# Kernel optimization log

Hardware: AMD Instinct MI355X
Metric: run time of the kernel (lower is better)

## Reference

```python
import jax, jax.numpy as jnp
import numpy as np

B, S, D, DK = 8, 2048, 768, 214
DROPOUT_P = 0.1


def setup_inputs() -> dict:
    key = jax.random.key(0)
    ks = jax.random.split(key, 11)
    x1 = jax.random.normal(ks[0], (B, S, D), jnp.float32)
    x2 = jax.random.normal(ks[1], (B, S, D), jnp.float32)
    x3 = jax.random.normal(ks[2], (B, S, D), jnp.float32)
    Wq = jax.random.normal(ks[3], (DK, D), jnp.float32) * (1.0 / np.sqrt(D))
    bq = jax.random.normal(ks[4], (DK,), jnp.float32) * 0.01
    Wk = jax.random.normal(ks[5], (DK, D), jnp.float32) * (1.0 / np.sqrt(D))
    bk = jax.random.normal(ks[6], (DK,), jnp.float32) * 0.01
    Wv = jax.random.normal(ks[7], (D, D), jnp.float32) * (1.0 / np.sqrt(D))
    bv = jax.random.normal(ks[8], (D,), jnp.float32) * 0.01
    # full-tensor elementwise divisor: uniform(0,1) + 1, as in the source
    inv_scale = jax.random.uniform(ks[9], (S, S), jnp.float32) + 1.0
    # deterministic inverted-dropout mask, keep prob = 1 - p
    keep = 1.0 - DROPOUT_P
    dropout_mask = (jax.random.uniform(ks[10], (B, S, S)) < keep).astype(jnp.float32) / keep
    return dict(x1=x1, x2=x2, x3=x3, Wq=Wq, bq=bq, Wk=Wk, bk=bk,
                Wv=Wv, bv=bv, inv_scale=inv_scale, dropout_mask=dropout_mask)


def reference(x1, x2, x3, Wq, bq, Wk, bk, Wv, bv, inv_scale, dropout_mask):
    q = jnp.einsum('bsd,kd->bsk', x1, Wq) + bq          # [B,S,DK]
    k = jnp.einsum('bsd,kd->bsk', x2, Wk) + bk          # [B,S,DK]
    v = jnp.einsum('bsd,ed->bse', x3, Wv) + bv          # [B,S,D]
    attn = jnp.einsum('bsk,btk->bst', q, k)             # [B,S,S]
    scaled = attn / inv_scale                           # elementwise full-tensor divisor
    p = jax.nn.softmax(scaled, axis=-1) * dropout_mask  # softmax + inverted dropout
    return jnp.einsum('bst,btd->bsd', p, v)             # [B,S,D]
```

## Files before the change

### kernel.cpp

```cpp
#include <hip/hip_runtime.h>
#include <hip/hip_bf16.h>

typedef unsigned short ushort;
typedef short bf16x8 __attribute__((ext_vector_type(8)));
typedef float f32x4 __attribute__((ext_vector_type(4)));

#define NB 8
#define SS 2048
#define DD 768
#define DKV 214
#define DKP 224
#define WROWS 256
#define MSHIFT 40.0f

__device__ __forceinline__ float bf2f(ushort u) {
  union { unsigned int i; float f; } v; v.i = ((unsigned int)u) << 16; return v.f;
}
__device__ __forceinline__ ushort f2bf(float f) {
  union { float f; unsigned int i; } v; v.f = f;
  unsigned int x = v.i;
  return (ushort)((x + 0x7fffu + ((x >> 16) & 1u)) >> 16);
}
__device__ __forceinline__ void split8v(f32x4 a, f32x4 b, bf16x8& h, bf16x8& l) {
#pragma unroll
  for (int j = 0; j < 4; ++j) {
    ushort h0 = f2bf(a[j]); h[j]     = (short)h0; l[j]     = (short)f2bf(a[j] - bf2f(h0));
    ushort h1 = f2bf(b[j]); h[j + 4] = (short)h1; l[j + 4] = (short)f2bf(b[j] - bf2f(h1));
  }
}
__device__ __forceinline__ bf16x8 cvt8v(f32x4 a, f32x4 b) {
  bf16x8 r;
#pragma unroll
  for (int j = 0; j < 4; ++j) { r[j] = (short)f2bf(a[j]); r[j + 4] = (short)f2bf(b[j]); }
  return r;
}
__device__ __forceinline__ void gload16(const void* g, void* l) {
  __builtin_amdgcn_global_load_lds(
      (const __attribute__((address_space(1))) void*)g,
      (__attribute__((address_space(3))) void*)l, 16, 0, 0);
}

__global__ __launch_bounds__(256)
void prep_w(const float* __restrict__ Wq, const float* __restrict__ Wk,
            const float* __restrict__ Wv,
            ushort* __restrict__ Wqh, ushort* __restrict__ Wql,
            ushort* __restrict__ Wkh, ushort* __restrict__ Wkl,
            ushort* __restrict__ Wvb, float* __restrict__ Z)
{
  const int NW = WROWS * DD;
  const int NV = DD * DD;
  for (int i = blockIdx.x * 256 + threadIdx.x; i < NB * SS; i += gridDim.x * 256)
    Z[i] = 0.f;
  for (int i = blockIdx.x * 256 + threadIdx.x; i < 2 * NW + NV; i += gridDim.x * 256) {
    if (i < NW) {
      int r = i / DD, c = i % DD;
      float v = (r < DKV) ? Wq[i] : 0.f;
      ushort h = f2bf(v);
      int d = (c >> 5) * (WROWS * 32) + r * 32 + (c & 31);
      Wqh[d] = h; Wql[d] = f2bf(v - bf2f(h));
    } else if (i < 2 * NW) {
      int j = i - NW;
      int r = j / DD, c = j % DD;
      float v = (r < DKV) ? Wk[j] : 0.f;
      ushort h = f2bf(v);
      int d = (c >> 5) * (WROWS * 32) + r * 32 + (c & 31);
      Wkh[d] = h; Wkl[d] = f2bf(v - bf2f(h));
    } else {
      int j = i - 2 * NW;
      int r = j / DD, c = j % DD;
      Wvb[(c >> 5) * (DD * 32) + r * 32 + (c & 31)] = f2bf(Wv[j]);
    }
  }
}

__global__ __launch_bounds__(256, 4)
void gemm_qk(const float* __restrict__ x1, const float* __restrict__ x2,
             const ushort* __restrict__ Wqh, const ushort* __restrict__ Wql,
             const ushort* __restrict__ Wkh, const ushort* __restrict__ Wkl,
             const float* __restrict__ bq, const float* __restrict__ bk,
             ushort* __restrict__ Qph, ushort* __restrict__ Qpl,
             ushort* __restrict__ Kph, ushort* __restrict__ Kpl)
{
  const int m0 = blockIdx.x * 64;
  const int which = blockIdx.y >> 1;
  const int n0 = (blockIdx.y & 1) * 128;
  const int tid = threadIdx.x;
  const int w  = tid >> 6;
  const int l  = tid & 63;
  const int lr = l & 15;
  const int lh = l >> 4;

  const float*  A    = which ? x2 : x1;
  const ushort* Bh   = which ? Wkh : Wqh;
  const ushort* Bl   = which ? Wkl : Wql;
  const float*  bias = which ? bk : bq;
  ushort* Ch = which ? Kph : Qph;
  ushort* Cl = which ? Kpl : Qpl;

  __shared__ __align__(16) char lds[2][2][128][64];

  const int srow = (w << 4) + (l >> 2);
  const size_t gc = (size_t)srow * 64 + (size_t)((((l & 3) ^ ((srow >> 1) & 3))) << 4);
  const char* gbh = (const char*)Bh + (size_t)n0 * 64;
  const char* gbl = (const char*)Bl + (size_t)n0 * 64;

  const f32x4 fzero = {0.f, 0.f, 0.f, 0.f};
  f32x4 acc[8];
#pragma unroll
  for (int nt = 0; nt < 8; ++nt) acc[nt] = fzero;

  const float* arow = A + (size_t)(m0 + w * 16 + lr) * DD + lh * 8;

#define QKSTAGE(buf, kk) do {                                             \
    size_t ko = (size_t)(kk) * (WROWS * 64);                              \
    gload16(gbh + ko + gc,        &lds[buf][0][w << 4][0]);               \
    gload16(gbh + ko + gc + 4096, &lds[buf][0][(w << 4) + 64][0]);        \
    gload16(gbl + ko + gc,        &lds[buf][1][w << 4][0]);               \
    gload16(gbl + ko + gc + 4096, &lds[buf][1][(w << 4) + 64][0]);        \
  } while (0)

  QKSTAGE(0, 0);
  f32x4 pa = *(const f32x4*)(arow);
  f32x4 pb = *(const f32x4*)(arow + 4);
  __syncthreads();

  for (int kk = 0; kk < 24; ++kk) {
    const int buf = kk & 1;
    if (kk < 23) QKSTAGE(buf ^ 1, kk + 1);
    f32x4 na = fzero, nb = fzero;
    if (kk < 23) {
      na = *(const f32x4*)(arow + (kk + 1) * 32);
      nb = *(const f32x4*)(arow + (kk + 1) * 32 + 4);
    }
    bf16x8 ah, al; split8v(pa, pb, ah, al);
#pragma unroll
    for (int nt = 0; nt < 8; ++nt) {
      int br = nt * 16 + lr;
      int bo = (lh ^ ((br >> 1) & 3)) << 4;
      bf16x8 wh = *(const bf16x8*)&lds[buf][0][br][bo];
      bf16x8 wl = *(const bf16x8*)&lds[buf][1][br][bo];
      acc[nt] = __builtin_amdgcn_mfma_f32_16x16x32_bf16(ah, wh, acc[nt], 0, 0, 0);
      acc[nt] = __builtin_amdgcn_mfma_f32_16x16x32_bf16(ah, wl, acc[nt], 0, 0, 0);
      acc[nt] = __builtin_amdgcn_mfma_f32_16x16x32_bf16(al, wh, acc[nt], 0, 0, 0);
    }
    __syncthreads();
    pa = na; pb = nb;
  }
#undef QKSTAGE

#pragma unroll
  for (int nt = 0; nt < 8; ++nt) {
    int n = n0 + nt * 16 + lr;
    if (n >= DKP) continue;
    float bv = (n < DKV) ? bias[n] : 0.f;
#pragma unroll
    for (int r = 0; r < 4; ++r) {
      int m = m0 + w * 16 + lh * 4 + r;
      int bb = m >> 11, s = m & 2047;
      float val = (n < DKV) ? (acc[nt][r] + bv) : 0.f;
      ushort h = f2bf(val);
      size_t idx = ((size_t)(bb * 7 + (n >> 5)) * SS + s) * 32 + (n & 31);
      Ch[idx] = h;
      Cl[idx] = f2bf(val - bf2f(h));
    }
  }
}

__global__ __launch_bounds__(256, 3)
void gemm_v(const float* __restrict__ A, const ushort* __restrict__ Bw,
            const float* __restrict__ bias, ushort* __restrict__ Vp)
{
  const int m0 = blockIdx.x * 64;
  const int n0 = blockIdx.y * 256;
  const int tid = threadIdx.x;
  const int w  = tid >> 6;
  const int l  = tid & 63;
  const int lr = l & 15;
  const int lh = l >> 4;

  __shared__ __align__(16) char smem[36864];
  typedef char VBuf[256][64];
  VBuf* stage = (VBuf*)smem;
  ushort (*lt)[72] = (ushort(*)[72])smem;

  const int srow = (w << 4) + (l >> 2);
  const size_t gc = (size_t)srow * 64 + (size_t)((((l & 3) ^ ((srow >> 1) & 3))) << 4);
  const char* gvw = (const char*)Bw + (size_t)n0 * 64;

  const f32x4 fzero = {0.f, 0.f, 0.f, 0.f};
  f32x4 acc[16];
#pragma unroll
  for (int nt = 0; nt < 16; ++nt) acc[nt] = fzero;

  const float* arow = A + (size_t)(m0 + w * 16 + lr) * DD + lh * 8;

#define VSTAGE(buf, kk) do {                                              \
    size_t ko = (size_t)(kk) * (DD * 64);                                 \
    gload16(gvw + ko + gc,         &stage[buf][w << 4][0]);               \
    gload16(gvw + ko + gc + 4096,  &stage[buf][(w << 4) + 64][0]);        \
    gload16(gvw + ko + gc + 8192,  &stage[buf][(w << 4) + 128][0]);       \
    gload16(gvw + ko + gc + 12288, &stage[buf][(w << 4) + 192][0]);       \
  } while (0)

  VSTAGE(0, 0);
  f32x4 pa = *(const f32x4*)(arow);
  f32x4 pb = *(const f32x4*)(arow + 4);
  __syncthreads();

  for (int kk = 0; kk < 24; ++kk) {
    const int buf = kk & 1;
    if (kk < 23) VSTAGE(buf ^ 1, kk + 1);
    f32x4 na = fzero, nb = fzero;
    if (kk < 23) {
      na = *(const f32x4*)(arow + (kk + 1) * 32);
      nb = *(const f32x4*)(arow + (kk + 1) * 32 + 4);
    }
    bf16x8 af = cvt8v(pa, pb);
#pragma unroll
    for (int nt = 0; nt < 16; ++nt) {
      int br = nt * 16 + lr;
      int bo = (lh ^ ((br >> 1) & 3)) << 4;
      bf16x8 bfr = *(const bf16x8*)&stage[buf][br][bo];
      acc[nt] = __builtin_amdgcn_mfma_f32_16x16x32_bf16(af, bfr, acc[nt], 0, 0, 0);
    }
    __syncthreads();
    pa = na; pb = nb;
  }
#undef VSTAGE

#pragma unroll
  for (int nt = 0; nt < 16; ++nt) {
    int nl = nt * 16 + lr;
    float bv = bias[n0 + nl];
#pragma unroll
    for (int r = 0; r < 4; ++r)
      lt[nl][w * 16 + lh * 4 + r] = f2bf(acc[nt][r] + bv);
  }
  __syncthreads();
  const int bb = m0 >> 11;
  const int s0 = m0 & 2047;
  for (int i = tid; i < 256 * 64; i += 256) {
    int nn = i >> 6, mm = i & 63;
    int d = n0 + nn, t = s0 + mm;
    Vp[((size_t)(bb * 64 + (t >> 5)) * DD + d) * 32 + (t & 31)] = lt[nn][mm];
  }
}

__global__ __launch_bounds__(512, 4)
void gemm_s(const ushort* __restrict__ Qph, const ushort* __restrict__ Qpl,
            const ushort* __restrict__ Kph, const ushort* __restrict__ Kpl,
            const float* __restrict__ isc, const float* __restrict__ dmask,
            ushort* __restrict__ Pp, float* __restrict__ Z)
{
  const int bid = blockIdx.x;
  const int bb = bid & 7;
  const int tt = bid >> 3;
  const int m0 = (tt & 15) * 128;
  const int n0 = (tt >> 4) * 128;
  const int tid = threadIdx.x;
  const int w  = tid >> 6;
  const int l  = tid & 63;
  const int lr = l & 15;
  const int lh = l >> 4;
  const int wm = w & 3;
  const int wn = w >> 2;

  __shared__ __align__(16) char lds[2][4][128][64];

  const int srow = (w << 4) + (l >> 2);
  const int ssl  = l & 3;
  const size_t gc = (size_t)srow * 64 + (size_t)((ssl ^ ((srow >> 1) & 3)) << 4);

  const char* gqh = (const char*)Qph + ((size_t)(bb * 7) * SS + m0) * 64;
  const char* gql = (const char*)Qpl + ((size_t)(bb * 7) * SS + m0) * 64;
  const char* gkh = (const char*)Kph + ((size_t)(bb * 7) * SS + n0) * 64;
  const char* gkl = (const char*)Kpl + ((size_t)(bb * 7) * SS + n0) * 64;

  const f32x4 fzero = {0.f, 0.f, 0.f, 0.f};
  f32x4 acc[2][4];
#pragma unroll
  for (int mf = 0; mf < 2; ++mf)
#pragma unroll
    for (int nf = 0; nf < 4; ++nf) acc[mf][nf] = fzero;

#define SSTAGE(buf, kk) do {                                            \
    size_t ko = (size_t)(kk) * (SS * 64);                               \
    gload16(gqh + ko + gc, &lds[buf][0][w << 4][0]);                    \
    gload16(gql + ko + gc, &lds[buf][1][w << 4][0]);                    \
    gload16(gkh + ko + gc, &lds[buf][2][w << 4][0]);                    \
    gload16(gkl + ko + gc, &lds[buf][3][w << 4][0]);                    \
  } while (0)

  SSTAGE(0, 0);
  __syncthreads();
#pragma unroll
  for (int t = 0; t < 7; ++t) {
    const int buf = t & 1;
    if (t < 6) SSTAGE(buf ^ 1, t + 1);
    bf16x8 ah[2], al[2];
#pragma unroll
    for (int mf = 0; mf < 2; ++mf) {
      int ar = wm * 32 + mf * 16 + lr;
      int ao = (lh ^ ((ar >> 1) & 3)) << 4;
      ah[mf] = *(const bf16x8*)&lds[buf][0][ar][ao];
      al[mf] = *(const bf16x8*)&lds[buf][1][ar][ao];
    }
#pragma unroll
    for (int nf = 0; nf < 4; ++nf) {
      int br = wn * 64 + nf * 16 + lr;
      int bo = (lh ^ ((br >> 1) & 3)) << 4;
      bf16x8 bh = *(const bf16x8*)&lds[buf][2][br][bo];
      bf16x8 bl = *(const bf16x8*)&lds[buf][3][br][bo];
#pragma unroll
      for (int mf = 0; mf < 2; ++mf) {
        acc[mf][nf] = __builtin_amdgcn_mfma_f32_16x16x32_bf16(ah[mf], bh, acc[mf][nf], 0, 0, 0);
        acc[mf][nf] = __builtin_amdgcn_mfma_f32_16x16x32_bf16(ah[mf], bl, acc[mf][nf], 0, 0, 0);
        acc[mf][nf] = __builtin_amdgcn_mfma_f32_16x16x32_bf16(al[mf], bh, acc[mf][nf], 0, 0, 0);
      }
    }
    __syncthreads();
  }
#undef SSTAGE

#pragma unroll
  for (int mf = 0; mf < 2; ++mf) {
#pragma unroll
    for (int r = 0; r < 4; ++r) {
      const int sr = m0 + wm * 32 + mf * 16 + lh * 4 + r;
      float z = 0.f;
#pragma unroll
      for (int nf = 0; nf < 4; ++nf) {
        const int tc = n0 + wn * 64 + nf * 16 + lr;
        float iv = isc[(size_t)sr * SS + tc];
        float sval = acc[mf][nf][r] * __builtin_amdgcn_rcpf(iv);
        float e = __expf(sval - MSHIFT);
        z += e;
        float mk = dmask[(size_t)bb * SS * SS + (size_t)sr * SS + tc];
        Pp[((size_t)(bb * 64 + (tc >> 5)) * SS + sr) * 32 + (tc & 31)] = f2bf(e * mk);
      }
#pragma unroll
      for (int off = 1; off < 16; off <<= 1) z += __shfl_xor(z, off);
      if (lr == 0) atomicAdd(&Z[bb * SS + sr], z);
    }
  }
}

__global__ __launch_bounds__(512, 4)
void gemm_pv(const ushort* __restrict__ Pp, const ushort* __restrict__ Vp,
             const float* __restrict__ Z, float* __restrict__ out)
{
  const int bid = blockIdx.x;
  const int bb = bid & 7;
  const int tt = bid >> 3;
  const int m0 = (tt & 15) * 128;
  const int n0 = (tt >> 4) * 128;
  const int tid = threadIdx.x;
  const int w  = tid >> 6;
  const int l  = tid & 63;
  const int lr = l & 15;
  const int lh = l >> 4;
  const int wm = w & 3;
  const int wn = w >> 2;

  __shared__ __align__(16) char lds[2][2][2][128][64];

  const int srow = (w << 4) + (l >> 2);
  const int ssl  = l & 3;
  const size_t gc = (size_t)srow * 64 + (size_t)((ssl ^ ((srow >> 1) & 3)) << 4);

  const char* gpb = (const char*)Pp + ((size_t)(bb * 64) * SS + m0) * 64;
  const char* gvb = (const char*)Vp + ((size_t)(bb * 64) * DD + n0) * 64;

  const f32x4 fzero = {0.f, 0.f, 0.f, 0.f};
  f32x4 acc[2][4];
#pragma unroll
  for (int mf = 0; mf < 2; ++mf)
#pragma unroll
    for (int nf = 0; nf < 4; ++nf) acc[mf][nf] = fzero;

#define PVSTAGE(buf, t) do {                                              \
    size_t k0 = (size_t)(t) * 2;                                          \
    gload16(gpb + k0 * (SS * 64) + gc,        &lds[buf][0][0][w << 4][0]); \
    gload16(gpb + (k0 + 1) * (SS * 64) + gc,  &lds[buf][0][1][w << 4][0]); \
    gload16(gvb + k0 * (DD * 64) + gc,        &lds[buf][1][0][w << 4][0]); \
    gload16(gvb + (k0 + 1) * (DD * 64) + gc,  &lds[buf][1][1][w << 4][0]); \
  } while (0)

  PVSTAGE(0, 0);
  __syncthreads();
  for (int t = 0; t < 32; ++t) {
    const int buf = t & 1;
    if (t < 31) PVSTAGE(buf ^ 1, t + 1);
#pragma unroll
    for (int pk = 0; pk < 2; ++pk) {
      bf16x8 af[2];
#pragma unroll
      for (int mf = 0; mf < 2; ++mf) {
        int ar = wm * 32 + mf * 16 + lr;
        int ao = (lh ^ ((ar >> 1) & 3)) << 4;
        af[mf] = *(const bf16x8*)&lds[buf][0][pk][ar][ao];
      }
#pragma unroll
      for (int nf = 0; nf < 4; ++nf) {
        int br = wn * 64 + nf * 16 + lr;
        int bo = (lh ^ ((br >> 1) & 3)) << 4;
        bf16x8 bfr = *(const bf16x8*)&lds[buf][1][pk][br][bo];
#pragma unroll
        for (int mf = 0; mf < 2; ++mf)
          acc[mf][nf] = __builtin_amdgcn_mfma_f32_16x16x32_bf16(af[mf], bfr, acc[mf][nf], 0, 0, 0);
      }
    }
    __syncthreads();
  }
#undef PVSTAGE

#pragma unroll
  for (int mf = 0; mf < 2; ++mf) {
#pragma unroll
    for (int r = 0; r < 4; ++r) {
      const int sr = m0 + wm * 32 + mf * 16 + lh * 4 + r;
      float rz = __builtin_amdgcn_rcpf(Z[bb * SS + sr]);
#pragma unroll
      for (int nf = 0; nf < 4; ++nf) {
        const int dc = n0 + wn * 64 + nf * 16 + lr;
        out[((size_t)bb * SS + sr) * DD + dc] = acc[mf][nf][r] * rz;
      }
    }
  }
}

extern "C" void kernel_launch(void* const* d_in, const int* in_sizes, int n_in,
                              void* d_out, int out_size, void* d_ws, size_t ws_size,
                              hipStream_t stream) {
  const float* x1  = (const float*)d_in[0];
  const float* x2  = (const float*)d_in[1];
  const float* x3  = (const float*)d_in[2];
  const float* Wq  = (const float*)d_in[3];
  const float* bq  = (const float*)d_in[4];
  const float* Wk  = (const float*)d_in[5];
  const float* bk  = (const float*)d_in[6];
  const float* Wv  = (const float*)d_in[7];
  const float* bv  = (const float*)d_in[8];
  const float* isc = (const float*)d_in[9];
  const float* dmk = (const float*)d_in[10];
  float* out = (float*)d_out;

  const size_t QKN = (size_t)NB * 7 * SS * 32;
  const size_t VPN = (size_t)NB * 64 * DD * 32;
  const size_t WN  = (size_t)WROWS * DD;
  const size_t NV  = (size_t)DD * DD;
  const size_t PPN = (size_t)NB * 64 * SS * 32;

  ushort* Qph = (ushort*)d_ws;
  ushort* Qpl = Qph + QKN;
  ushort* Kph = Qpl + QKN;
  ushort* Kpl = Kph + QKN;
  ushort* Vp  = Kpl + QKN;
  ushort* Wqh = Vp + VPN;
  ushort* Wql = Wqh + WN;
  ushort* Wkh = Wql + WN;
  ushort* Wkl = Wkh + WN;
  ushort* Wvb = Wkl + WN;
  ushort* Pp  = Wvb + NV;
  float*  Zb  = (float*)(Pp + PPN);

  dim3 blk(256);
  prep_w<<<dim3(512), blk, 0, stream>>>(Wq, Wk, Wv, Wqh, Wql, Wkh, Wkl, Wvb, Zb);
  gemm_qk<<<dim3(256, 4), blk, 0, stream>>>(x1, x2, Wqh, Wql, Wkh, Wkl, bq, bk,
                                            Qph, Qpl, Kph, Kpl);
  gemm_v <<<dim3(256, 3), blk, 0, stream>>>(x3, Wvb, bv, Vp);
  gemm_s <<<dim3(2048), dim3(512), 0, stream>>>(Qph, Qpl, Kph, Kpl, isc, dmk, Pp, Zb);
  gemm_pv<<<dim3(768),  dim3(512), 0, stream>>>(Pp, Vp, Zb, out);
}
```

Measured before the change: 283.5 us.

## Enlarge per-wave tiles in score and PV GEMMs, drop LDS double buffering

The score kernel now computes a 128x256 tile per block, with each of its 8 waves owning a 64x64 sub-tile. The PV kernel runs 4 waves per block, each owning a 64x64 sub-tile of a 128x128 tile. Each loaded LDS fragment now feeds more MFMAs, which cuts LDS traffic per flop and halves the score grid. The ping-pong LDS buffers are replaced by a single buffer with load-then-sync after each compute step. That removes the overlap between global loads and MFMA work, and the larger accumulator arrays raise register pressure.

```diff
diff --git a/kernel.cpp b/kernel.cpp
--- a/kernel.cpp
+++ b/kernel.cpp
@@ -256,20 +256,22 @@
   const int bb = bid & 7;
   const int tt = bid >> 3;
   const int m0 = (tt & 15) * 128;
-  const int n0 = (tt >> 4) * 128;
+  const int n0 = (tt >> 4) * 256;
   const int tid = threadIdx.x;
   const int w  = tid >> 6;
   const int l  = tid & 63;
   const int lr = l & 15;
   const int lh = l >> 4;
-  const int wm = w & 3;
-  const int wn = w >> 2;
-
-  __shared__ __align__(16) char lds[2][4][128][64];
+  const int wm = w & 1;
+  const int wn = w >> 1;
+
+  __shared__ __align__(16) char Qhb[128][64];
+  __shared__ __align__(16) char Qlb[128][64];
+  __shared__ __align__(16) char Khb[256][64];
+  __shared__ __align__(16) char Klb[256][64];
 
   const int srow = (w << 4) + (l >> 2);
-  const int ssl  = l & 3;
-  const size_t gc = (size_t)srow * 64 + (size_t)((ssl ^ ((srow >> 1) & 3)) << 4);
+  const size_t gc = (size_t)srow * 64 + (size_t)((((l & 3) ^ ((srow >> 1) & 3))) << 4);
 
   const char* gqh = (const char*)Qph + ((size_t)(bb * 7) * SS + m0) * 64;
   const char* gql = (const char*)Qpl + ((size_t)(bb * 7) * SS + m0) * 64;
@@ -277,56 +279,60 @@
   const char* gkl = (const char*)Kpl + ((size_t)(bb * 7) * SS + n0) * 64;
 
   const f32x4 fzero = {0.f, 0.f, 0.f, 0.f};
-  f32x4 acc[2][4];
-#pragma unroll
-  for (int mf = 0; mf < 2; ++mf)
+  f32x4 acc[4][4];
+#pragma unroll
+  for (int mf = 0; mf < 4; ++mf)
 #pragma unroll
     for (int nf = 0; nf < 4; ++nf) acc[mf][nf] = fzero;
 
-#define SSTAGE(buf, kk) do {                                            \
+#define SSTAGE(kk) do {                                                 \
     size_t ko = (size_t)(kk) * (SS * 64);                               \
-    gload16(gqh + ko + gc, &lds[buf][0][w << 4][0]);                    \
-    gload16(gql + ko + gc, &lds[buf][1][w << 4][0]);                    \
-    gload16(gkh + ko + gc, &lds[buf][2][w << 4][0]);                    \
-    gload16(gkl + ko + gc, &lds[buf][3][w << 4][0]);                    \
+    gload16(gqh + ko + gc,        &Qhb[w << 4][0]);                     \
+    gload16(gql + ko + gc,        &Qlb[w << 4][0]);                     \
+    gload16(gkh + ko + gc,        &Khb[w << 4][0]);                     \
+    gload16(gkh + ko + gc + 8192, &Khb[(w << 4) + 128][0]);             \
+    gload16(gkl + ko + gc,        &Klb[w << 4][0]);                     \
+    gload16(gkl + ko + gc + 8192, &Klb[(w << 4) + 128][0]);             \
   } while (0)
 
-  SSTAGE(0, 0);
+  SSTAGE(0);
   __syncthreads();
-#pragma unroll
+#pragma unroll 1
   for (int t = 0; t < 7; ++t) {
-    const int buf = t & 1;
-    if (t < 6) SSTAGE(buf ^ 1, t + 1);
-    bf16x8 ah[2], al[2];
-#pragma unroll
-    for (int mf = 0; mf < 2; ++mf) {
-      int ar = wm * 32 + mf * 16 + lr;
-      int ao = (lh ^ ((ar >> 1) & 3)) << 4;
-      ah[mf] = *(const bf16x8*)&lds[buf][0][ar][ao];
-      al[mf] = *(const bf16x8*)&lds[buf][1][ar][ao];
-    }
+    bf16x8 bh[4], bl[4];
 #pragma unroll
     for (int nf = 0; nf < 4; ++nf) {
       int br = wn * 64 + nf * 16 + lr;
       int bo = (lh ^ ((br >> 1) & 3)) << 4;
-      bf16x8 bh = *(const bf16x8*)&lds[buf][2][br][bo];
-      bf16x8 bl = *(const bf16x8*)&lds[buf][3][br][bo];
-#pragma unroll
-      for (int mf = 0; mf < 2; ++mf) {
-        acc[mf][nf] = __builtin_amdgcn_mfma_f32_16x16x32_bf16(ah[mf], bh, acc[mf][nf], 0, 0, 0);
-        acc[mf][nf] = __builtin_amdgcn_mfma_f32_16x16x32_bf16(ah[mf], bl, acc[mf][nf], 0, 0, 0);
-        acc[mf][nf] = __builtin_amdgcn_mfma_f32_16x16x32_bf16(al[mf], bh, acc[mf][nf], 0, 0, 0);
+      bh[nf] = *(const bf16x8*)&Khb[br][bo];
+      bl[nf] = *(const bf16x8*)&Klb[br][bo];
+    }
+#pragma unroll
+    for (int mf = 0; mf < 4; ++mf) {
+      int ar = wm * 64 + mf * 16 + lr;
+      int ao = (lh ^ ((ar >> 1) & 3)) << 4;
+      bf16x8 ah = *(const bf16x8*)&Qhb[ar][ao];
+      bf16x8 al = *(const bf16x8*)&Qlb[ar][ao];
+#pragma unroll
+      for (int nf = 0; nf < 4; ++nf) {
+        acc[mf][nf] = __builtin_amdgcn_mfma_f32_16x16x32_bf16(ah, bh[nf], acc[mf][nf], 0, 0, 0);
+        acc[mf][nf] = __builtin_amdgcn_mfma_f32_16x16x32_bf16(ah, bl[nf], acc[mf][nf], 0, 0, 0);
+        acc[mf][nf] = __builtin_amdgcn_mfma_f32_16x16x32_bf16(al, bh[nf], acc[mf][nf], 0, 0, 0);
       }
     }
     __syncthreads();
+    if (t < 6) {
+      SSTAGE(t + 1);
+      __syncthreads();
+    }
   }
 #undef SSTAGE
 
 #pragma unroll
-  for (int mf = 0; mf < 2; ++mf) {
+  for (int mf = 0; mf < 4; ++mf) {
 #pragma unroll
     for (int r = 0; r < 4; ++r) {
-      const int sr = m0 + wm * 32 + mf * 16 + lh * 4 + r;
+      const int sr = m0 + wm * 64 + mf * 16 + lh * 4 + r;
       float z = 0.f;
 #pragma unroll
       for (int nf = 0; nf < 4; ++nf) {
@@ -345,7 +351,7 @@
   }
 }
 
-__global__ __launch_bounds__(512, 4)
+__global__ __launch_bounds__(256, 4)
 void gemm_pv(const ushort* __restrict__ Pp, const ushort* __restrict__ Vp,
              const float* __restrict__ Z, float* __restrict__ out)
 {
@@ -359,66 +365,73 @@
   const int l  = tid & 63;
   const int lr = l & 15;
   const int lh = l >> 4;
-  const int wm = w & 3;
-  const int wn = w >> 2;
-
-  __shared__ __align__(16) char lds[2][2][2][128][64];
+  const int wm = w & 1;
+  const int wn = w >> 1;
+
+  __shared__ __align__(16) char Plb[2][128][64];
+  __shared__ __align__(16) char Vlb[2][128][64];
 
   const int srow = (w << 4) + (l >> 2);
-  const int ssl  = l & 3;
-  const size_t gc = (size_t)srow * 64 + (size_t)((ssl ^ ((srow >> 1) & 3)) << 4);
+  const size_t gc = (size_t)srow * 64 + (size_t)((((l & 3) ^ ((srow >> 1) & 3))) << 4);
 
   const char* gpb = (const char*)Pp + ((size_t)(bb * 64) * SS + m0) * 64;
   const char* gvb = (const char*)Vp + ((size_t)(bb * 64) * DD + n0) * 64;
 
   const f32x4 fzero = {0.f, 0.f, 0.f, 0.f};
-  f32x4 acc[2][4];
-#pragma unroll
-  for (int mf = 0; mf < 2; ++mf)
+  f32x4 acc[4][4];
+#pragma unroll
+  for (int mf = 0; mf < 4; ++mf)
 #pragma unroll
     for (int nf = 0; nf < 4; ++nf) acc[mf][nf] = fzero;
 
-#define PVSTAGE(buf, t) do {                                              \
+#define PVSTAGE(t) do {                                                   \
     size_t k0 = (size_t)(t) * 2;                                          \
-    gload16(gpb + k0 * (SS * 64) + gc,        &lds[buf][0][0][w << 4][0]); \
-    gload16(gpb + (k0 + 1) * (SS * 64) + gc,  &lds[buf][0][1][w << 4][0]); \
-    gload16(gvb + k0 * (DD * 64) + gc,        &lds[buf][1][0][w << 4][0]); \
-    gload16(gvb + (k0 + 1) * (DD * 64) + gc,  &lds[buf][1][1][w << 4][0]); \
+    gload16(gpb + k0 * (SS * 64) + gc,              &Plb[0][w << 4][0]);  \
+    gload16(gpb + k0 * (SS * 64) + gc + 4096,       &Plb[0][(w << 4) + 64][0]); \
+    gload16(gpb + (k0 + 1) * (SS * 64) + gc,        &Plb[1][w << 4][0]);  \
+    gload16(gpb + (k0 + 1) * (SS * 64) + gc + 4096, &Plb[1][(w << 4) + 64][0]); \
+    gload16(gvb + k0 * (DD * 64) + gc,              &Vlb[0][w << 4][0]);  \
+    gload16(gvb + k0 * (DD * 64) + gc + 4096,       &Vlb[0][(w << 4) + 64][0]); \
+    gload16(gvb + (k0 + 1) * (DD * 64) + gc,        &Vlb[1][w << 4][0]);  \
+    gload16(gvb + (k0 + 1) * (DD * 64) + gc + 4096, &Vlb[1][(w << 4) + 64][0]); \
   } while (0)
 
-  PVSTAGE(0, 0);
+  PVSTAGE(0);
   __syncthreads();
+#pragma unroll 1
   for (int t = 0; t < 32; ++t) {
-    const int buf = t & 1;
-    if (t < 31) PVSTAGE(buf ^ 1, t + 1);
 #pragma unroll
     for (int pk = 0; pk < 2; ++pk) {
-      bf16x8 af[2];
-#pragma unroll
-      for (int mf = 0; mf < 2; ++mf) {
-        int ar = wm * 32 + mf * 16 + lr;
-        int ao = (lh ^ ((ar >> 1) & 3)) << 4;
-        af[mf] = *(const bf16x8*)&lds[buf][0][pk][ar][ao];
-      }
+      bf16x8 bfr[4];
 #pragma unroll
       for (int nf = 0; nf < 4; ++nf) {
         int br = wn * 64 + nf * 16 + lr;
         int bo = (lh ^ ((br >> 1) & 3)) << 4;
-        bf16x8 bfr = *(const bf16x8*)&lds[buf][1][pk][br][bo];
-#pragma unroll
-        for (int mf = 0; mf < 2; ++mf)
-          acc[mf][nf] = __builtin_amdgcn_mfma_f32_16x16x32_bf16(af[mf], bfr, acc[mf][nf], 0, 0, 0);
+        bfr[nf] = *(const bf16x8*)&Vlb[pk][br][bo];
       }
+#pragma unroll
+      for (int mf = 0; mf < 4; ++mf) {
+        int ar = wm * 64 + mf * 16 + lr;
+        int ao = (lh ^ ((ar >> 1) & 3)) << 4;
+        bf16x8 af = *(const bf16x8*)&Plb[pk][ar][ao];
+#pragma unroll
+        for (int nf = 0; nf < 4; ++nf)
+          acc[mf][nf] = __builtin_amdgcn_mfma_f32_16x16x32_bf16(af, bfr[nf], acc[mf][nf], 0, 0, 0);
+      }
     }
     __syncthreads();
+    if (t < 31) {
+      PVSTAGE(t + 1);
+      __syncthreads();
+    }
   }
 #undef PVSTAGE
 
 #pragma unroll
-  for (int mf = 0; mf < 2; ++mf) {
+  for (int mf = 0; mf < 4; ++mf) {
 #pragma unroll
     for (int r = 0; r < 4; ++r) {
-      const int sr = m0 + wm * 32 + mf * 16 + lh * 4 + r;
+      const int sr = m0 + wm * 64 + mf * 16 + lh * 4 + r;
       float rz = __builtin_amdgcn_rcpf(Z[bb * SS + sr]);
 #pragma unroll
       for (int nf = 0; nf < 4; ++nf) {
@@ -469,6 +482,6 @@
   gemm_qk<<<dim3(256, 4), blk, 0, stream>>>(x1, x2, Wqh, Wql, Wkh, Wkl, bq, bk,
                                             Qph, Qpl, Kph, Kpl);
   gemm_v <<<dim3(256, 3), blk, 0, stream>>>(x3, Wvb, bv, Vp);
-  gemm_s <<<dim3(2048), dim3(512), 0, stream>>>(Qph, Qpl, Kph, Kpl, isc, dmk, Pp, Zb);
-  gemm_pv<<<dim3(768),  dim3(512), 0, stream>>>(Pp, Vp, Zb, out);
-}
+  gemm_s <<<dim3(1024), dim3(512), 0, stream>>>(Qph, Qpl, Kph, Kpl, isc, dmk, Pp, Zb);
+  gemm_pv<<<dim3(768),  dim3(256), 0, stream>>>(Pp, Vp, Zb, out);
+}
```

After: 273.6 us. 1.04x faster.
